# Kernel tuning notes

Measured on AMD Instinct MI355X. Metric: run time of the kernel, lower is better.

The kernel has to match this reference:

```python
import jax, jax.numpy as jnp
import numpy as np

N_NODES = 50000
N_EDGES = 800000
IN_DIM = 256
HID = 64
LAT = 64
HEADS = 4
NUM_GRAPHS = 64
NEG_SLOPE = 0.2


def _gat_layer(h_in, src, dst, W, a_s, a_d, b, heads, concat):
    N = h_in.shape[0]
    F_ = W.shape[1] // heads
    h = (h_in @ W).reshape(N, heads, F_)              # [N,H,F]
    al_s = jnp.sum(h * a_s, axis=-1)                  # [N,H]
    al_d = jnp.sum(h * a_d, axis=-1)                  # [N,H]
    e = jax.nn.leaky_relu(al_s[src] + al_d[dst], NEG_SLOPE)  # [E,H]
    # scatter-softmax over edges grouped by destination node
    m = jax.ops.segment_max(e, dst, num_segments=N)
    e = jnp.exp(e - m[dst])
    s = jax.ops.segment_sum(e, dst, num_segments=N)
    alpha = e / (s[dst] + 1e-16)                      # [E,H]
    out = jax.ops.segment_sum(h[src] * alpha[:, :, None], dst, num_segments=N)
    out = out.reshape(N, heads * F_) if concat else out.mean(axis=1)
    return out + b


def setup_inputs() -> dict:
    key = jax.random.key(0)
    ks = jax.random.split(key, 20)
    g = lambda k, shp, sc: jax.random.normal(k, shp, jnp.float32) * sc
    inp = {}
    inp['x'] = g(ks[0], (N_NODES, IN_DIM), 1.0)
    inp['edge_index'] = jax.random.randint(ks[1], (2, N_EDGES), 0, N_NODES, jnp.int32)
    inp['batch'] = jnp.sort(jax.random.randint(ks[2], (N_NODES,), 0, NUM_GRAPHS, jnp.int32))
    # layer 0: IN_DIM -> HID, 4 heads, concat
    inp['W1'] = g(ks[3], (IN_DIM, HEADS * HID), 0.05)
    inp['a1s'] = g(ks[4], (HEADS, HID), 0.05)
    inp['a1d'] = g(ks[5], (HEADS, HID), 0.05)
    inp['b1'] = jnp.zeros((HEADS * HID,), jnp.float32)
    # layer 1: 4*HID -> HID, 4 heads, concat
    inp['W2'] = g(ks[6], (HEADS * HID, HEADS * HID), 0.05)
    inp['a2s'] = g(ks[7], (HEADS, HID), 0.05)
    inp['a2d'] = g(ks[8], (HEADS, HID), 0.05)
    inp['b2'] = jnp.zeros((HEADS * HID,), jnp.float32)
    # layer 2: 4*HID -> LAT, 1 head, mean
    inp['W3'] = g(ks[9], (HEADS * HID, LAT), 0.05)
    inp['a3s'] = g(ks[10], (1, LAT), 0.05)
    inp['a3d'] = g(ks[11], (1, LAT), 0.05)
    inp['b3'] = jnp.zeros((LAT,), jnp.float32)
    # VAE head
    inp['Wmu'] = g(ks[12], (LAT, LAT), 0.1)
    inp['bmu'] = jnp.zeros((LAT,), jnp.float32)
    inp['Wlv'] = g(ks[13], (LAT, LAT), 0.1)
    inp['blv'] = jnp.zeros((LAT,), jnp.float32)
    return inp


def reference(x, edge_index, batch, W1, a1s, a1d, b1, W2, a2s, a2d, b2,
              W3, a3s, a3d, b3, Wmu, bmu, Wlv, blv):
    N = x.shape[0]
    loop = jnp.arange(N, dtype=edge_index.dtype)
    src = jnp.concatenate([edge_index[0], loop])   # add self-loops (PyG default)
    dst = jnp.concatenate([edge_index[1], loop])
    h = _gat_layer(x, src, dst, W1, a1s, a1d, b1, HEADS, True)
    h = jax.nn.elu(h)
    h = _gat_layer(h, src, dst, W2, a2s, a2d, b2, HEADS, True)
    h = jax.nn.elu(h)
    h = _gat_layer(h, src, dst, W3, a3s, a3d, b3, 1, False)
    # global mean pool per graph
    sums = jax.ops.segment_sum(h, batch, num_segments=NUM_GRAPHS)
    cnts = jax.ops.segment_sum(jnp.ones((N,), h.dtype), batch, num_segments=NUM_GRAPHS)
    pooled = sums / jnp.maximum(cnts, 1.0)[:, None]  # [G, LAT]
    mu = pooled @ Wmu + bmu
    logvar = pooled @ Wlv + blv
    std = jnp.exp(0.5 * logvar)
    eps = jax.random.normal(jax.random.key(42), std.shape, std.dtype)
    z = mu + eps * std
    return (mu, logvar, z)
```

## Files before the change

### kernel.cpp

```cpp
#include <hip/hip_runtime.h>
#include <hip/hip_bf16.h>
#include <cstdint>
#include <math.h>


#define N_NODES 50000
#define N_EDGES 800000
#define NEG_SLOPE 0.2f
#define CAP 128

typedef __hip_bfloat16 bf16;
typedef short short8 __attribute__((ext_vector_type(8)));
typedef float floatx4 __attribute__((ext_vector_type(4)));
typedef float floatx2 __attribute__((ext_vector_type(2)));

__device__ __forceinline__ float bf2f(bf16 v){ return __bfloat162float(v); }
__device__ __forceinline__ float bflo(unsigned u){ union{unsigned u; float f;} c; c.u = u<<16; return c.f; }
__device__ __forceinline__ float bfhi(unsigned u){ union{unsigned u; float f;} c; c.u = u & 0xFFFF0000u; return c.f; }
__device__ __forceinline__ float leaky(float v){ return v>0.f ? v : NEG_SLOPE*v; }
__device__ __forceinline__ unsigned short f2bu(float f){
  union{ bf16 b; unsigned short u; } c; c.b = __float2bfloat16(f); return c.u;
}
__device__ __forceinline__ unsigned char f2fp8(float v){
  int p = __builtin_amdgcn_cvt_pk_fp8_f32(v, v, 0, false);
  return (unsigned char)(p & 0xff);
}
__device__ __forceinline__ void acc_fp8x4(float* acc, unsigned wrd, float wgt){
  floatx2 lo = __builtin_amdgcn_cvt_pk_f32_fp8((int)wrd, false);
  floatx2 hi = __builtin_amdgcn_cvt_pk_f32_fp8((int)wrd, true);
  acc[0] = fmaf(lo[0], wgt, acc[0]);
  acc[1] = fmaf(lo[1], wgt, acc[1]);
  acc[2] = fmaf(hi[0], wgt, acc[2]);
  acc[3] = fmaf(hi[1], wgt, acc[3]);
}

__device__ __forceinline__ void tf_round(unsigned& x0, unsigned& x1, int r){
  x0 += x1; x1 = (x1<<r)|(x1>>(32-r)); x1 ^= x0;
}
__device__ __forceinline__ void threefry2x32(unsigned k0, unsigned k1, unsigned& x0, unsigned& x1){
  unsigned ks2 = k0 ^ k1 ^ 0x1BD11BDAu;
  x0 += k0; x1 += k1;
  tf_round(x0,x1,13); tf_round(x0,x1,15); tf_round(x0,x1,26); tf_round(x0,x1,6);
  x0 += k1; x1 += ks2 + 1u;
  tf_round(x0,x1,17); tf_round(x0,x1,29); tf_round(x0,x1,16); tf_round(x0,x1,24);
  x0 += ks2; x1 += k0 + 2u;
  tf_round(x0,x1,13); tf_round(x0,x1,15); tf_round(x0,x1,26); tf_round(x0,x1,6);
  x0 += k0; x1 += k1 + 3u;
  tf_round(x0,x1,17); tf_round(x0,x1,29); tf_round(x0,x1,16); tf_round(x0,x1,24);
  x0 += k1; x1 += ks2 + 4u;
  tf_round(x0,x1,13); tf_round(x0,x1,15); tf_round(x0,x1,26); tf_round(x0,x1,6);
  x0 += ks2; x1 += k0 + 5u;
}

__device__ __forceinline__ float erfinv_approx(float x){
  float w = -log1pf(-x*x);
  float p;
  if (w < 5.0f){
    w = w - 2.5f;
    p = 2.81022636e-08f;
    p = fmaf(p,w,3.43273939e-07f);
    p = fmaf(p,w,-3.5233877e-06f);
    p = fmaf(p,w,-4.39150654e-06f);
    p = fmaf(p,w,0.00021858087f);
    p = fmaf(p,w,-0.00125372503f);
    p = fmaf(p,w,-0.00417768164f);
    p = fmaf(p,w,0.246640727f);
    p = fmaf(p,w,1.50140941f);
  } else {
    w = sqrtf(w) - 3.0f;
    p = -0.000200214257f;
    p = fmaf(p,w,0.000100950558f);
    p = fmaf(p,w,0.00134934322f);
    p = fmaf(p,w,-0.00367342844f);
    p = fmaf(p,w,0.00573950773f);
    p = fmaf(p,w,-0.0076224613f);
    p = fmaf(p,w,0.00943887047f);
    p = fmaf(p,w,1.00167406f);
    p = fmaf(p,w,2.83297682f);
  }
  return p*x;
}

__global__ __launch_bounds__(256) void wt_all_kernel(
        const float* __restrict__ W1, const float* __restrict__ W2,
        const float* __restrict__ W3, short* __restrict__ Wt1,
        short* __restrict__ Wt2, short* __restrict__ Wt3){
  const float* W; short* Wt; int Nn;
  if (blockIdx.z == 0){ W = W1; Wt = Wt1; Nn = 256; }
  else if (blockIdx.z == 1){ W = W2; Wt = Wt2; Nn = 256; }
  else { W = W3; Wt = Wt3; Nn = 64; }
  const int n0 = blockIdx.x*32, k0 = blockIdx.y*32;
  if (n0 >= Nn) return;
  __shared__ float tile[32][33];
  const int tx = threadIdx.x & 31, ty = threadIdx.x >> 5;
  #pragma unroll
  for (int i=0;i<4;++i)
    tile[ty+8*i][tx] = W[(size_t)(k0+ty+8*i)*Nn + n0 + tx];
  __syncthreads();
  #pragma unroll
  for (int i=0;i<4;++i)
    Wt[(size_t)(n0+ty+8*i)*256 + k0 + tx] = (short)f2bu(tile[tx][ty+8*i]);
}

template<int OUT, bool INBF>
__global__ __launch_bounds__(256) void gemm_mfma_kernel(const void* __restrict__ inp,
        const short* __restrict__ Wt, void* __restrict__ outv,
        const float* __restrict__ a_s, const float* __restrict__ a_d,
        float* __restrict__ als, float* __restrict__ ald, int N){
  constexpr int M_BLK = (OUT==256) ? 64 : 256;
  constexpr int H = (OUT==256) ? 4 : 1;
  __shared__ short As[M_BLK*48];
  __shared__ short Bs[OUT*48];
  const int t = threadIdx.x;
  const int w = t>>6, lane = t&63;
  const int lm = lane&15, g = lane>>4;
  const int m0 = blockIdx.x * M_BLK;
  const int m_off = (OUT==256) ? 0 : w*64;
  const int n0    = (OUT==256) ? w*64 : 0;

  floatx4 acc[4][4] = {};

  for (int kk=0; kk<8; ++kk){
    const int k0 = kk*32;
    __syncthreads();
    for (int a = t; a < M_BLK*4; a += 256){
      int r = a>>2, c = a&3;
      int gr = m0 + r;
      uint4 v = make_uint4(0u,0u,0u,0u);
      if (gr < N){
        if constexpr (INBF){
          v = *(const uint4*)((const bf16*)inp + (size_t)gr*256 + k0 + c*8);
        } else {
          const float* p = (const float*)inp + (size_t)gr*256 + k0 + c*8;
          float4 f0 = *(const float4*)p;
          float4 f1 = *(const float4*)(p+4);
          v.x = (unsigned)f2bu(f0.x) | ((unsigned)f2bu(f0.y)<<16);
          v.y = (unsigned)f2bu(f0.z) | ((unsigned)f2bu(f0.w)<<16);
          v.z = (unsigned)f2bu(f1.x) | ((unsigned)f2bu(f1.y)<<16);
          v.w = (unsigned)f2bu(f1.z) | ((unsigned)f2bu(f1.w)<<16);
        }
      }
      *(uint4*)&As[r*48 + c*8] = v;
    }
    for (int a = t; a < OUT*4; a += 256){
      int r = a>>2, c = a&3;
      uint4 v = *(const uint4*)(Wt + (size_t)r*256 + k0 + c*8);
      *(uint4*)&Bs[r*48 + c*8] = v;
    }
    __syncthreads();
    short8 af[4], bfr[4];
    #pragma unroll
    for (int mt=0;mt<4;++mt)
      af[mt] = *(const short8*)&As[(m_off + mt*16 + lm)*48 + g*8];
    #pragma unroll
    for (int nt=0;nt<4;++nt)
      bfr[nt] = *(const short8*)&Bs[(n0 + nt*16 + lm)*48 + g*8];
    #pragma unroll
    for (int mt=0;mt<4;++mt)
      #pragma unroll
      for (int nt=0;nt<4;++nt)
        acc[mt][nt] = __builtin_amdgcn_mfma_f32_16x16x32_bf16(af[mt], bfr[nt], acc[mt][nt], 0, 0, 0);
  }

  float asv[4], adv[4];
  #pragma unroll
  for (int nt=0;nt<4;++nt){
    asv[nt] = a_s[n0 + nt*16 + lm];
    adv[nt] = a_d[n0 + nt*16 + lm];
  }
  const int head = (OUT==256) ? w : 0;
  #pragma unroll
  for (int mt=0;mt<4;++mt){
    #pragma unroll
    for (int reg=0;reg<4;++reg){
      int gr = m0 + m_off + mt*16 + g*4 + reg;
      bool valid = gr < N;
      float ps = 0.f, pd = 0.f;
      #pragma unroll
      for (int nt=0;nt<4;++nt){
        float v = acc[mt][nt][reg];
        if (valid){
          if constexpr (OUT==256){
            ((unsigned char*)outv)[(size_t)gr*256 + n0 + nt*16 + lm] = f2fp8(v);
          } else {
            ((bf16*)outv)[(size_t)gr*OUT + n0 + nt*16 + lm] = __float2bfloat16(v);
          }
        }
        ps = fmaf(v, asv[nt], ps);
        pd = fmaf(v, adv[nt], pd);
      }
      #pragma unroll
      for (int o=1;o<16;o<<=1){ ps += __shfl_xor(ps,o); pd += __shfl_xor(pd,o); }
      if (lm==0 && valid){
        als[gr*H + head] = ps;
        ald[gr*H + head] = pd;
      }
    }
  }
}

__global__ void build_kernel(const int* __restrict__ ei, int* __restrict__ deg,
        unsigned short* __restrict__ csr, int E, int N){
  int e = blockIdx.x*blockDim.x+threadIdx.x;
  if (e >= E+N) return;
  int s_ = (e < E) ? ei[e]   : e-E;
  int d_ = (e < E) ? ei[E+e] : e-E;
  int r = atomicAdd(&deg[d_], 1);
  if (r < CAP) csr[(size_t)d_*CAP + r] = (unsigned short)s_;
}

template<bool ELU>
__global__ __launch_bounds__(256) void aggregate4_kernel(const unsigned char* __restrict__ h8,
        const float* __restrict__ als, const float* __restrict__ ald,
        const int* __restrict__ deg, const unsigned short* __restrict__ csr,
        const float* __restrict__ bias, bf16* __restrict__ out){
  __shared__ int   s_src[4][64];
  __shared__ float s_w[4][64][4];
  const int wv_ = threadIdx.x >> 6;
  const int n = blockIdx.x*4 + wv_;
  if (n >= N_NODES) return;
  const int lane = threadIdx.x & 63;
  const int r = lane>>4;
  const int f = lane&15;
  const int head = f>>2;
  const int p0 = n*CAP;
  const int cnt = min(deg[n], CAP);
  const float4 aldn4 = *(const float4*)(ald + n*4);
  float ssum = 0.f;
  float acc[16] = {};
  for (int c=0; c<cnt; c+=64){
    int e = c + lane;
    int src = n; float4 w4 = make_float4(0.f,0.f,0.f,0.f);
    if (e < cnt){
      src = (int)csr[p0+e];
      float4 av = *(const float4*)(als + src*4);
      w4.x = expf(leaky(av.x + aldn4.x));
      w4.y = expf(leaky(av.y + aldn4.y));
      w4.z = expf(leaky(av.z + aldn4.z));
      w4.w = expf(leaky(av.w + aldn4.w));
    }
    s_src[wv_][lane] = src;
    *(float4*)&s_w[wv_][lane][0] = w4;
    int ce = min(64, cnt - c);
    int cp = (ce+7)&~7;
    for (int i=0;i<cp;i+=8){
      int src0 = s_src[wv_][i+r], src1 = s_src[wv_][i+4+r];
      float w0 = s_w[wv_][i+r][head], w1 = s_w[wv_][i+4+r][head];
      uint4 h0 = *(const uint4*)(h8 + (size_t)src0*256 + f*16);
      uint4 h1 = *(const uint4*)(h8 + (size_t)src1*256 + f*16);
      ssum += w0 + w1;
      acc_fp8x4(acc+0,  h0.x, w0); acc_fp8x4(acc+4,  h0.y, w0);
      acc_fp8x4(acc+8,  h0.z, w0); acc_fp8x4(acc+12, h0.w, w0);
      acc_fp8x4(acc+0,  h1.x, w1); acc_fp8x4(acc+4,  h1.y, w1);
      acc_fp8x4(acc+8,  h1.z, w1); acc_fp8x4(acc+12, h1.w, w1);
    }
  }
  #pragma unroll
  for (int j=0;j<16;++j){
    acc[j] += __shfl_xor(acc[j], 16);
    acc[j] += __shfl_xor(acc[j], 32);
  }
  ssum += __shfl_xor(ssum, 16);
  ssum += __shfl_xor(ssum, 32);
  if (r==0){
    float inv = 1.f/(ssum + 1e-16f);
    #pragma unroll
    for (int half=0; half<2; ++half){
      float4 b0 = *(const float4*)(bias + f*16 + half*8);
      float4 b1 = *(const float4*)(bias + f*16 + half*8 + 4);
      float rv[8];
      rv[0]=acc[half*8+0]*inv+b0.x; rv[1]=acc[half*8+1]*inv+b0.y;
      rv[2]=acc[half*8+2]*inv+b0.z; rv[3]=acc[half*8+3]*inv+b0.w;
      rv[4]=acc[half*8+4]*inv+b1.x; rv[5]=acc[half*8+5]*inv+b1.y;
      rv[6]=acc[half*8+6]*inv+b1.z; rv[7]=acc[half*8+7]*inv+b1.w;
      union{ bf16 b[8]; uint4 u; } pk;
      #pragma unroll
      for (int j=0;j<8;++j){
        float v = rv[j];
        if (ELU) v = (v>0.f)?v:expm1f(v);
        pk.b[j] = __float2bfloat16(v);
      }
      *(uint4*)(out + (size_t)n*256 + f*16 + half*8) = pk.u;
    }
  }
}

__global__ __launch_bounds__(256) void aggregate1_kernel(const bf16* __restrict__ h,
        const float* __restrict__ als, const float* __restrict__ ald,
        const int* __restrict__ deg, const unsigned short* __restrict__ csr,
        const float* __restrict__ bias, bf16* __restrict__ out){
  __shared__ int   s_src[4][64];
  __shared__ float s_w[4][64];
  const int wv_ = threadIdx.x >> 6;
  const int n = blockIdx.x*4 + wv_;
  if (n >= N_NODES) return;
  const int lane = threadIdx.x & 63;
  const int r = lane>>4;
  const int f = lane&15;
  const int p0 = n*CAP;
  const int cnt = min(deg[n], CAP);
  const float aldn = ald[n];
  float ssum = 0.f;
  float acc[4] = {};
  for (int c=0; c<cnt; c+=64){
    int e = c + lane;
    int src = n; float wv = 0.f;
    if (e < cnt){
      src = (int)csr[p0+e];
      wv = expf(leaky(als[src] + aldn));
    }
    s_src[wv_][lane] = src; s_w[wv_][lane] = wv;
    int ce = min(64, cnt - c);
    int cp = (ce+7)&~7;
    for (int i=0;i<cp;i+=8){
      int src0 = s_src[wv_][i+r], src1 = s_src[wv_][i+4+r];
      float w0 = s_w[wv_][i+r],   w1 = s_w[wv_][i+4+r];
      uint2 h0 = *(const uint2*)(h + (size_t)src0*64 + f*4);
      uint2 h1 = *(const uint2*)(h + (size_t)src1*64 + f*4);
      ssum += w0 + w1;
      acc[0]=fmaf(bflo(h0.x),w0,acc[0]); acc[1]=fmaf(bfhi(h0.x),w0,acc[1]);
      acc[2]=fmaf(bflo(h0.y),w0,acc[2]); acc[3]=fmaf(bfhi(h0.y),w0,acc[3]);
      acc[0]=fmaf(bflo(h1.x),w1,acc[0]); acc[1]=fmaf(bfhi(h1.x),w1,acc[1]);
      acc[2]=fmaf(bflo(h1.y),w1,acc[2]); acc[3]=fmaf(bfhi(h1.y),w1,acc[3]);
    }
  }
  #pragma unroll
  for (int j=0;j<4;++j){
    acc[j] += __shfl_xor(acc[j], 16);
    acc[j] += __shfl_xor(acc[j], 32);
  }
  ssum += __shfl_xor(ssum, 16);
  ssum += __shfl_xor(ssum, 32);
  if (r==0){
    float inv = 1.f/(ssum + 1e-16f);
    union{ bf16 b[4]; uint2 u; } pk;
    #pragma unroll
    for (int j=0;j<4;++j) pk.b[j] = __float2bfloat16(acc[j]*inv + bias[f*4+j]);
    *(uint2*)(out + (size_t)n*64 + f*4) = pk.u;
  }
}

__global__ __launch_bounds__(64) void pool_kernel(const bf16* __restrict__ h3,
        const int* __restrict__ batch, float* __restrict__ psum, float* __restrict__ pcnt,
        int N, int chunk){
  int n0 = blockIdx.x*chunk;
  if (n0 >= N) return;
  int n1 = min(N, n0+chunk);
  int t = threadIdx.x;
  int gcur = batch[n0];
  float acc = 0.f, cnt = 0.f;
  for (int n=n0; n<n1; ++n){
    int g = batch[n];
    if (g != gcur){
      atomicAdd(&psum[gcur*64+t], acc);
      if (t==0) atomicAdd(&pcnt[gcur], cnt);
      acc = 0.f; cnt = 0.f; gcur = g;
    }
    acc += bf2f(h3[(size_t)n*64+t]);
    cnt += 1.f;
  }
  atomicAdd(&psum[gcur*64+t], acc);
  if (t==0) atomicAdd(&pcnt[gcur], cnt);
}

__global__ __launch_bounds__(64) void head_kernel(const float* __restrict__ psum,
        const float* __restrict__ pcnt,
        const float* __restrict__ Wmu, const float* __restrict__ bmu,
        const float* __restrict__ Wlv, const float* __restrict__ blv,
        float* __restrict__ out){
  int g = blockIdx.x, t = threadIdx.x;
  __shared__ float p[64];
  float cnt = fmaxf(pcnt[g], 1.0f);
  p[t] = psum[g*64+t] / cnt;
  __syncthreads();
  float mu = bmu[t], lv = blv[t];
  for (int k=0;k<64;++k){
    float pk = p[k];
    mu = fmaf(pk, Wmu[(size_t)k*64+t], mu);
    lv = fmaf(pk, Wlv[(size_t)k*64+t], lv);
  }
  int i = g*64 + t;
  unsigned x0 = 0u, x1 = (unsigned)i;
  threefry2x32(0u, 42u, x0, x1);
  unsigned bits = x0 ^ x1;
  float f = __uint_as_float((bits>>9) | 0x3F800000u) - 1.0f;
  const float lo = __uint_as_float(0xBF7FFFFFu);
  float u = fmaxf(lo, f*2.0f + lo);
  float eps = 1.41421356f * erfinv_approx(u);
  float z = mu + eps * expf(0.5f*lv);
  out[i]        = mu;
  out[4096 + i] = lv;
  out[8192 + i] = z;
}

extern "C" void kernel_launch(void* const* d_in, const int* in_sizes, int n_in,
                              void* d_out, int out_size, void* d_ws, size_t ws_size,
                              hipStream_t stream){
  const float* x    = (const float*)d_in[0];
  const int*   ei   = (const int*)d_in[1];
  const int*   batch= (const int*)d_in[2];
  const float* W1   = (const float*)d_in[3];
  const float* a1s  = (const float*)d_in[4];
  const float* a1d  = (const float*)d_in[5];
  const float* b1   = (const float*)d_in[6];
  const float* W2   = (const float*)d_in[7];
  const float* a2s  = (const float*)d_in[8];
  const float* a2d  = (const float*)d_in[9];
  const float* b2   = (const float*)d_in[10];
  const float* W3   = (const float*)d_in[11];
  const float* a3s  = (const float*)d_in[12];
  const float* a3d  = (const float*)d_in[13];
  const float* b3   = (const float*)d_in[14];
  const float* Wmu  = (const float*)d_in[15];
  const float* bmu  = (const float*)d_in[16];
  const float* Wlv  = (const float*)d_in[17];
  const float* blv  = (const float*)d_in[18];
  float* out = (float*)d_out;

  const int N = N_NODES, E = N_EDGES;
  const int ET = E + N;

  char* ws = (char*)d_ws;
  size_t o = 0;
  auto alloc = [&](size_t bytes)->void*{
    void* p = ws + o; o += (bytes + 255) & ~(size_t)255; return p;
  };
  bf16*  hA      = (bf16*) alloc((size_t)N*256*2);
  unsigned char* hB8 = (unsigned char*)alloc((size_t)N*256);
  bf16*  h3      = (bf16*) alloc((size_t)N*64*2);
  float* als     = (float*)alloc((size_t)N*4*4);
  float* ald     = (float*)alloc((size_t)N*4*4);
  int*   deg     = (int*)  alloc((size_t)N*4);
  unsigned short* csr16 = (unsigned short*)alloc((size_t)N*CAP*2);
  short* Wt1     = (short*)alloc(256*256*2);
  short* Wt2     = (short*)alloc(256*256*2);
  short* Wt3     = (short*)alloc(64*256*2);
  float* psum    = (float*)alloc(64*64*4 + 64*4);
  float* pcnt    = psum + 64*64;
  (void)ws_size; (void)n_in; (void)in_sizes; (void)out_size;

  const int TB = 256;

  wt_all_kernel<<<dim3(8,8,3), 256, 0, stream>>>(W1, W2, W3, Wt1, Wt2, Wt3);

  hipMemsetAsync(deg, 0, (size_t)N*4, stream);
  build_kernel<<<(ET+TB-1)/TB, TB, 0, stream>>>(ei, deg, csr16, E, N);

  gemm_mfma_kernel<256,false><<<(N+63)/64, 256, 0, stream>>>(x, Wt1, hB8, a1s, a1d, als, ald, N);
  aggregate4_kernel<true><<<(N+3)/4, 256, 0, stream>>>(hB8, als, ald, deg, csr16, b1, hA);

  gemm_mfma_kernel<256,true><<<(N+63)/64, 256, 0, stream>>>(hA, Wt2, hB8, a2s, a2d, als, ald, N);
  aggregate4_kernel<true><<<(N+3)/4, 256, 0, stream>>>(hB8, als, ald, deg, csr16, b2, hA);

  gemm_mfma_kernel<64,true><<<(N+255)/256, 256, 0, stream>>>(hA, Wt3, h3, a3s, a3d, als, ald, N);
  aggregate1_kernel<<<(N+3)/4, 256, 0, stream>>>(h3, als, ald, deg, csr16, b3, hA);

  hipMemsetAsync(psum, 0, 64*64*4 + 64*4, stream);
  const int PBLK = 512;
  const int chunk = (N + PBLK - 1)/PBLK;
  pool_kernel<<<PBLK, 64, 0, stream>>>(hA, batch, psum, pcnt, N, chunk);
  head_kernel<<<64, 64, 0, stream>>>(psum, pcnt, Wmu, bmu, Wlv, blv, out);
}
```

Baseline: 420.1 us.

## Store fp8 features head-major and split 4-head aggregation into per-head passes

The GEMM epilogue now writes the fp8 feature table as four head-major slabs (one 64-byte row per node per head) instead of one 256-byte row per node. The 4-head aggregation launches four times as many blocks, each handling one head. Each wave processes 16 edges per step with 4 lanes per 64-byte row. The aim is to shrink the working set each pass gathers from so it fits better in cache, and to raise parallelism per node. The cost is reading the CSR and attention logits four times and doing a longer shuffle reduction.

```diff
diff --git a/kernel.cpp b/kernel.cpp
--- a/kernel.cpp
+++ b/kernel.cpp
@@ -8,6 +8,7 @@
 #define N_EDGES 800000
 #define NEG_SLOPE 0.2f
 #define CAP 128
+#define NB4 12500
 
 typedef __hip_bfloat16 bf16;
 typedef short short8 __attribute__((ext_vector_type(8)));
@@ -181,7 +182,7 @@
         float v = acc[mt][nt][reg];
         if (valid){
           if constexpr (OUT==256){
-            ((unsigned char*)outv)[(size_t)gr*256 + n0 + nt*16 + lm] = f2fp8(v);
+            ((unsigned char*)outv)[((size_t)head*N + gr)*64 + nt*16 + lm] = f2fp8(v);
           } else {
             ((bf16*)outv)[(size_t)gr*OUT + n0 + nt*16 + lm] = __float2bfloat16(v);
           }
@@ -210,44 +211,43 @@
 }
 
 template<bool ELU>
-__global__ __launch_bounds__(256) void aggregate4_kernel(const unsigned char* __restrict__ h8,
+__global__ __launch_bounds__(256) void aggregate4s_kernel(const unsigned char* __restrict__ h8s,
         const float* __restrict__ als, const float* __restrict__ ald,
         const int* __restrict__ deg, const unsigned short* __restrict__ csr,
         const float* __restrict__ bias, bf16* __restrict__ out){
   __shared__ int   s_src[4][64];
-  __shared__ float s_w[4][64][4];
+  __shared__ float s_w[4][64];
+  const int b = (int)blockIdx.x;
+  const int s = b / NB4;
+  const int nb = b - s*NB4;
   const int wv_ = threadIdx.x >> 6;
-  const int n = blockIdx.x*4 + wv_;
+  const int n = nb*4 + wv_;
   if (n >= N_NODES) return;
   const int lane = threadIdx.x & 63;
-  const int r = lane>>4;
-  const int f = lane&15;
-  const int head = f>>2;
+  const int r = lane>>2;
+  const int f = lane&3;
   const int p0 = n*CAP;
   const int cnt = min(deg[n], CAP);
-  const float4 aldn4 = *(const float4*)(ald + n*4);
+  const float aldn = ald[n*4 + s];
+  const unsigned char* tbl = h8s + (size_t)s*N_NODES*64;
   float ssum = 0.f;
   float acc[16] = {};
   for (int c=0; c<cnt; c+=64){
     int e = c + lane;
-    int src = n; float4 w4 = make_float4(0.f,0.f,0.f,0.f);
+    int src = n; float wgt = 0.f;
     if (e < cnt){
       src = (int)csr[p0+e];
-      float4 av = *(const float4*)(als + src*4);
-      w4.x = expf(leaky(av.x + aldn4.x));
-      w4.y = expf(leaky(av.y + aldn4.y));
-      w4.z = expf(leaky(av.z + aldn4.z));
-      w4.w = expf(leaky(av.w + aldn4.w));
+      wgt = expf(leaky(als[src*4 + s] + aldn));
     }
     s_src[wv_][lane] = src;
-    *(float4*)&s_w[wv_][lane][0] = w4;
+    s_w[wv_][lane] = wgt;
     int ce = min(64, cnt - c);
-    int cp = (ce+7)&~7;
-    for (int i=0;i<cp;i+=8){
-      int src0 = s_src[wv_][i+r], src1 = s_src[wv_][i+4+r];
-      float w0 = s_w[wv_][i+r][head], w1 = s_w[wv_][i+4+r][head];
-      uint4 h0 = *(const uint4*)(h8 + (size_t)src0*256 + f*16);
-      uint4 h1 = *(const uint4*)(h8 + (size_t)src1*256 + f*16);
+    int cp = (ce+31)&~31;
+    for (int i=0;i<cp;i+=32){
+      int src0 = s_src[wv_][i+r], src1 = s_src[wv_][i+16+r];
+      float w0 = s_w[wv_][i+r],   w1 = s_w[wv_][i+16+r];
+      uint4 h0 = *(const uint4*)(tbl + (size_t)src0*64 + f*16);
+      uint4 h1 = *(const uint4*)(tbl + (size_t)src1*64 + f*16);
       ssum += w0 + w1;
       acc_fp8x4(acc+0,  h0.x, w0); acc_fp8x4(acc+4,  h0.y, w0);
       acc_fp8x4(acc+8,  h0.z, w0); acc_fp8x4(acc+12, h0.w, w0);
@@ -257,17 +257,22 @@
   }
   #pragma unroll
   for (int j=0;j<16;++j){
+    acc[j] += __shfl_xor(acc[j], 4);
+    acc[j] += __shfl_xor(acc[j], 8);
     acc[j] += __shfl_xor(acc[j], 16);
     acc[j] += __shfl_xor(acc[j], 32);
   }
+  ssum += __shfl_xor(ssum, 4);
+  ssum += __shfl_xor(ssum, 8);
   ssum += __shfl_xor(ssum, 16);
   ssum += __shfl_xor(ssum, 32);
   if (r==0){
     float inv = 1.f/(ssum + 1e-16f);
+    const float* bp = bias + s*64 + f*16;
     #pragma unroll
     for (int half=0; half<2; ++half){
-      float4 b0 = *(const float4*)(bias + f*16 + half*8);
-      float4 b1 = *(const float4*)(bias + f*16 + half*8 + 4);
+      float4 b0 = *(const float4*)(bp + half*8);
+      float4 b1 = *(const float4*)(bp + half*8 + 4);
       float rv[8];
       rv[0]=acc[half*8+0]*inv+b0.x; rv[1]=acc[half*8+1]*inv+b0.y;
       rv[2]=acc[half*8+2]*inv+b0.z; rv[3]=acc[half*8+3]*inv+b0.w;
@@ -280,7 +285,7 @@
         if (ELU) v = (v>0.f)?v:expm1f(v);
         pk.b[j] = __float2bfloat16(v);
       }
-      *(uint4*)(out + (size_t)n*256 + f*16 + half*8) = pk.u;
+      *(uint4*)(out + (size_t)n*256 + s*64 + f*16 + half*8) = pk.u;
     }
   }
 }
@@ -447,10 +452,10 @@
   build_kernel<<<(ET+TB-1)/TB, TB, 0, stream>>>(ei, deg, csr16, E, N);
 
   gemm_mfma_kernel<256,false><<<(N+63)/64, 256, 0, stream>>>(x, Wt1, hB8, a1s, a1d, als, ald, N);
-  aggregate4_kernel<true><<<(N+3)/4, 256, 0, stream>>>(hB8, als, ald, deg, csr16, b1, hA);
+  aggregate4s_kernel<true><<<4*NB4, 256, 0, stream>>>(hB8, als, ald, deg, csr16, b1, hA);
 
   gemm_mfma_kernel<256,true><<<(N+63)/64, 256, 0, stream>>>(hA, Wt2, hB8, a2s, a2d, als, ald, N);
-  aggregate4_kernel<true><<<(N+3)/4, 256, 0, stream>>>(hB8, als, ald, deg, csr16, b2, hA);
+  aggregate4s_kernel<true><<<4*NB4, 256, 0, stream>>>(hB8, als, ald, deg, csr16, b2, hA);
 
   gemm_mfma_kernel<64,true><<<(N+255)/256, 256, 0, stream>>>(hA, Wt3, h3, a3s, a3d, als, ald, N);
   aggregate1_kernel<<<(N+3)/4, 256, 0, stream>>>(h3, als, ald, deg, csr16, b3, hA);
```

Result: slower. 623.4 us (+48.4%).

## Unroll edge gather loops by four and fuse mean-pool into final aggregation

Applied to the files above, without the earlier changes.

Doubles the per-iteration edge unroll in both aggregation kernels so more independent gathers are in flight. Folds global mean pooling into the last aggregation kernel via per-node atomic adds into the pooled sums, removing the intermediate layer-3 output buffer and the separate pool launch. Risks heavy atomic contention on the small pooled buffer and extra padded work for low-degree nodes.

```diff
diff --git a/kernel.cpp b/kernel.cpp
--- a/kernel.cpp
+++ b/kernel.cpp
@@ -242,17 +242,25 @@
     s_src[wv_][lane] = src;
     *(float4*)&s_w[wv_][lane][0] = w4;
     int ce = min(64, cnt - c);
-    int cp = (ce+7)&~7;
-    for (int i=0;i<cp;i+=8){
-      int src0 = s_src[wv_][i+r], src1 = s_src[wv_][i+4+r];
-      float w0 = s_w[wv_][i+r][head], w1 = s_w[wv_][i+4+r][head];
+    int cp = (ce+15)&~15;
+    for (int i=0;i<cp;i+=16){
+      int src0 = s_src[wv_][i+r],    src1 = s_src[wv_][i+4+r];
+      int src2 = s_src[wv_][i+8+r],  src3 = s_src[wv_][i+12+r];
+      float w0 = s_w[wv_][i+r][head],    w1 = s_w[wv_][i+4+r][head];
+      float w2 = s_w[wv_][i+8+r][head],  w3 = s_w[wv_][i+12+r][head];
       uint4 h0 = *(const uint4*)(h8 + (size_t)src0*256 + f*16);
       uint4 h1 = *(const uint4*)(h8 + (size_t)src1*256 + f*16);
-      ssum += w0 + w1;
+      uint4 h2 = *(const uint4*)(h8 + (size_t)src2*256 + f*16);
+      uint4 h3 = *(const uint4*)(h8 + (size_t)src3*256 + f*16);
+      ssum += (w0 + w1) + (w2 + w3);
       acc_fp8x4(acc+0,  h0.x, w0); acc_fp8x4(acc+4,  h0.y, w0);
       acc_fp8x4(acc+8,  h0.z, w0); acc_fp8x4(acc+12, h0.w, w0);
       acc_fp8x4(acc+0,  h1.x, w1); acc_fp8x4(acc+4,  h1.y, w1);
       acc_fp8x4(acc+8,  h1.z, w1); acc_fp8x4(acc+12, h1.w, w1);
+      acc_fp8x4(acc+0,  h2.x, w2); acc_fp8x4(acc+4,  h2.y, w2);
+      acc_fp8x4(acc+8,  h2.z, w2); acc_fp8x4(acc+12, h2.w, w2);
+      acc_fp8x4(acc+0,  h3.x, w3); acc_fp8x4(acc+4,  h3.y, w3);
+      acc_fp8x4(acc+8,  h3.z, w3); acc_fp8x4(acc+12, h3.w, w3);
     }
   }
   #pragma unroll
@@ -285,10 +293,11 @@
   }
 }
 
-__global__ __launch_bounds__(256) void aggregate1_kernel(const bf16* __restrict__ h,
+__global__ __launch_bounds__(256) void aggregate1_pool_kernel(const bf16* __restrict__ h,
         const float* __restrict__ als, const float* __restrict__ ald,
         const int* __restrict__ deg, const unsigned short* __restrict__ csr,
-        const float* __restrict__ bias, bf16* __restrict__ out){
+        const float* __restrict__ bias, const int* __restrict__ batch,
+        float* __restrict__ psum, float* __restrict__ pcnt){
   __shared__ int   s_src[4][64];
   __shared__ float s_w[4][64];
   const int wv_ = threadIdx.x >> 6;
@@ -311,17 +320,25 @@
     }
     s_src[wv_][lane] = src; s_w[wv_][lane] = wv;
     int ce = min(64, cnt - c);
-    int cp = (ce+7)&~7;
-    for (int i=0;i<cp;i+=8){
-      int src0 = s_src[wv_][i+r], src1 = s_src[wv_][i+4+r];
+    int cp = (ce+15)&~15;
+    for (int i=0;i<cp;i+=16){
+      int src0 = s_src[wv_][i+r],   src1 = s_src[wv_][i+4+r];
+      int src2 = s_src[wv_][i+8+r], src3 = s_src[wv_][i+12+r];
       float w0 = s_w[wv_][i+r],   w1 = s_w[wv_][i+4+r];
+      float w2 = s_w[wv_][i+8+r], w3 = s_w[wv_][i+12+r];
       uint2 h0 = *(const uint2*)(h + (size_t)src0*64 + f*4);
       uint2 h1 = *(const uint2*)(h + (size_t)src1*64 + f*4);
-      ssum += w0 + w1;
+      uint2 h2 = *(const uint2*)(h + (size_t)src2*64 + f*4);
+      uint2 h3 = *(const uint2*)(h + (size_t)src3*64 + f*4);
+      ssum += (w0 + w1) + (w2 + w3);
       acc[0]=fmaf(bflo(h0.x),w0,acc[0]); acc[1]=fmaf(bfhi(h0.x),w0,acc[1]);
       acc[2]=fmaf(bflo(h0.y),w0,acc[2]); acc[3]=fmaf(bfhi(h0.y),w0,acc[3]);
       acc[0]=fmaf(bflo(h1.x),w1,acc[0]); acc[1]=fmaf(bfhi(h1.x),w1,acc[1]);
       acc[2]=fmaf(bflo(h1.y),w1,acc[2]); acc[3]=fmaf(bfhi(h1.y),w1,acc[3]);
+      acc[0]=fmaf(bflo(h2.x),w2,acc[0]); acc[1]=fmaf(bfhi(h2.x),w2,acc[1]);
+      acc[2]=fmaf(bflo(h2.y),w2,acc[2]); acc[3]=fmaf(bfhi(h2.y),w2,acc[3]);
+      acc[0]=fmaf(bflo(h3.x),w3,acc[0]); acc[1]=fmaf(bfhi(h3.x),w3,acc[1]);
+      acc[2]=fmaf(bflo(h3.y),w3,acc[2]); acc[3]=fmaf(bfhi(h3.y),w3,acc[3]);
     }
   }
   #pragma unroll
@@ -333,34 +350,12 @@
   ssum += __shfl_xor(ssum, 32);
   if (r==0){
     float inv = 1.f/(ssum + 1e-16f);
-    union{ bf16 b[4]; uint2 u; } pk;
-    #pragma unroll
-    for (int j=0;j<4;++j) pk.b[j] = __float2bfloat16(acc[j]*inv + bias[f*4+j]);
-    *(uint2*)(out + (size_t)n*64 + f*4) = pk.u;
-  }
-}
-
-__global__ __launch_bounds__(64) void pool_kernel(const bf16* __restrict__ h3,
-        const int* __restrict__ batch, float* __restrict__ psum, float* __restrict__ pcnt,
-        int N, int chunk){
-  int n0 = blockIdx.x*chunk;
-  if (n0 >= N) return;
-  int n1 = min(N, n0+chunk);
-  int t = threadIdx.x;
-  int gcur = batch[n0];
-  float acc = 0.f, cnt = 0.f;
-  for (int n=n0; n<n1; ++n){
     int g = batch[n];
-    if (g != gcur){
-      atomicAdd(&psum[gcur*64+t], acc);
-      if (t==0) atomicAdd(&pcnt[gcur], cnt);
-      acc = 0.f; cnt = 0.f; gcur = g;
-    }
-    acc += bf2f(h3[(size_t)n*64+t]);
-    cnt += 1.f;
-  }
-  atomicAdd(&psum[gcur*64+t], acc);
-  if (t==0) atomicAdd(&pcnt[gcur], cnt);
+    float* pg = psum + g*64 + f*4;
+    #pragma unroll
+    for (int j=0;j<4;++j) atomicAdd(&pg[j], acc[j]*inv + bias[f*4+j]);
+    if (f==0 && lane==0) atomicAdd(&pcnt[g], 1.0f);
+  }
 }
 
 __global__ __launch_bounds__(64) void head_kernel(const float* __restrict__ psum,
@@ -446,6 +441,8 @@
   hipMemsetAsync(deg, 0, (size_t)N*4, stream);
   build_kernel<<<(ET+TB-1)/TB, TB, 0, stream>>>(ei, deg, csr16, E, N);
 
+  hipMemsetAsync(psum, 0, 64*64*4 + 64*4, stream);
+
   gemm_mfma_kernel<256,false><<<(N+63)/64, 256, 0, stream>>>(x, Wt1, hB8, a1s, a1d, als, ald, N);
   aggregate4_kernel<true><<<(N+3)/4, 256, 0, stream>>>(hB8, als, ald, deg, csr16, b1, hA);
 
@@ -453,11 +450,7 @@
   aggregate4_kernel<true><<<(N+3)/4, 256, 0, stream>>>(hB8, als, ald, deg, csr16, b2, hA);
 
   gemm_mfma_kernel<64,true><<<(N+255)/256, 256, 0, stream>>>(hA, Wt3, h3, a3s, a3d, als, ald, N);
-  aggregate1_kernel<<<(N+3)/4, 256, 0, stream>>>(h3, als, ald, deg, csr16, b3, hA);
-
-  hipMemsetAsync(psum, 0, 64*64*4 + 64*4, stream);
-  const int PBLK = 512;
-  const int chunk = (N + PBLK - 1)/PBLK;
-  pool_kernel<<<PBLK, 64, 0, stream>>>(hA, batch, psum, pcnt, N, chunk);
+  aggregate1_pool_kernel<<<(N+3)/4, 256, 0, stream>>>(h3, als, ald, deg, csr16, b3, batch, psum, pcnt);
+
   head_kernel<<<64, 64, 0, stream>>>(psum, pcnt, Wmu, bmu, Wlv, blv, out);
 }
```

Result: slower. 796.6 us (+89.6%).
